# Kernel optimization log

Measured on AMD Instinct MI355X. Metric: run time of the kernel, lower is better.

The kernel has to match this reference:

```python
import jax, jax.numpy as jnp
import numpy as np

EMBED_DIM = 512
NUM_HEADS = 8
HEAD_DIM = EMBED_DIM // NUM_HEADS
B, S = 4, 2048


def setup_inputs() -> dict:
    key = jax.random.key(0)
    ks = jax.random.split(key, 9)
    scale = 1.0 / np.sqrt(EMBED_DIM)
    def lin(k):
        kw, kb = jax.random.split(k)
        W = jax.random.uniform(kw, (EMBED_DIM, EMBED_DIM), jnp.float32, -scale, scale)
        b = jax.random.uniform(kb, (EMBED_DIM,), jnp.float32, -scale, scale)
        return W, b
    Wq, bq = lin(ks[0])
    Wk, bk = lin(ks[1])
    Wv, bv = lin(ks[2])
    Wo, bo = lin(ks[3])
    x = jax.random.normal(ks[4], (B, S, EMBED_DIM), jnp.float32)
    return {"x": x, "Wq": Wq, "bq": bq, "Wk": Wk, "bk": bk,
            "Wv": Wv, "bv": bv, "Wo": Wo, "bo": bo}


def reference(x, Wq, bq, Wk, bk, Wv, bv, Wo, bo):
    # x: [B, S, E]. Linear uses y = x @ W^T + b (torch convention: W stored [out,in]).
    def split_heads(t):
        return t.reshape(B, S, NUM_HEADS, HEAD_DIM).transpose(0, 2, 1, 3)  # [B,H,S,D]
    q = split_heads(x @ Wq.T + bq)
    k = split_heads(x @ Wk.T + bk)
    v = split_heads(x @ Wv.T + bv)
    scores = jnp.einsum('bhsd,bhtd->bhst', q, k) / jnp.sqrt(jnp.float32(HEAD_DIM))
    attn_weights = jax.nn.softmax(scores, axis=-1)  # dropout is identity in eval mode
    attn_output = jnp.einsum('bhst,bhtd->bhsd', attn_weights, v)
    attn_output = attn_output.transpose(0, 2, 1, 3).reshape(B, S, EMBED_DIM)
    output = attn_output @ Wo.T + bo
    return output, attn_weights
```

## Files before the change

### kernel.cpp

```cpp
#include <hip/hip_runtime.h>
#include <stdint.h>

#define NB 4
#define NH 8
#define SS 2048
#define EE 512
#define DD 64
#define MM (NB*SS)
#define LDP 72
#define LDW 136

typedef __attribute__((ext_vector_type(8))) __bf16 bf16x8;
typedef __attribute__((ext_vector_type(8))) unsigned short ushort8;
typedef __attribute__((ext_vector_type(4))) unsigned short ushort4v;
typedef __attribute__((ext_vector_type(4))) float f32x4;

__device__ __forceinline__ uint16_t f2bf(float f) {
    union { float f; uint32_t u; } v; v.f = f;
    return (uint16_t)((v.u + 0x7fffu + ((v.u >> 16) & 1u)) >> 16);
}
__device__ __forceinline__ float bf2f(uint16_t h) {
    union { uint32_t u; float f; } v; v.u = ((uint32_t)h) << 16;
    return v.f;
}

__global__ __launch_bounds__(256) void split_all(
        const float* __restrict__ x,  const float* __restrict__ Wq,
        const float* __restrict__ Wk, const float* __restrict__ Wv,
        const float* __restrict__ Wo,
        uint16_t* __restrict__ xh, uint16_t* __restrict__ xl,
        uint16_t* __restrict__ wqkvh, uint16_t* __restrict__ wqkvl,
        uint16_t* __restrict__ woh, uint16_t* __restrict__ wol)
{
    const int tid = threadIdx.x;
    int b = blockIdx.x;
    const float* src; uint16_t* dh; uint16_t* dl; int i;
    if (b < 4096) { src = x; dh = xh; dl = xl; i = b*256 + tid; }
    else {
        b -= 4096;
        const int seg = b >> 8;
        i = (b & 255)*256 + tid;
        src = (seg == 0) ? Wq : (seg == 1) ? Wk : (seg == 2) ? Wv : Wo;
        if (seg < 3) { dh = wqkvh + (size_t)seg*262144; dl = wqkvl + (size_t)seg*262144; }
        else         { dh = woh; dl = wol; }
    }
    f32x4 v = reinterpret_cast<const f32x4*>(src)[i];
    ushort4v h, l;
#pragma unroll
    for (int j = 0; j < 4; j++) {
        uint16_t hh = f2bf(v[j]);
        h[j] = hh;
        l[j] = f2bf(v[j] - bf2f(hh));
    }
    reinterpret_cast<ushort4v*>(dh)[i] = h;
    reinterpret_cast<ushort4v*>(dl)[i] = l;
}

__global__ __launch_bounds__(256, 3)
void gemm_qkv(const uint16_t* __restrict__ Ah, const uint16_t* __restrict__ Al,
              const uint16_t* __restrict__ Bh, const uint16_t* __restrict__ Bl,
              const float* __restrict__ bq, const float* __restrict__ bk,
              const float* __restrict__ bv, float qscale,
              uint16_t* __restrict__ qh, uint16_t* __restrict__ ql,
              uint16_t* __restrict__ kh, uint16_t* __restrict__ kl,
              uint16_t* __restrict__ vh)
{
    __shared__ uint16_t sAh[64*64], sAl[64*64], sBh[128*64], sBl[128*64];
    const int t = threadIdx.x;
    const int lane = t & 63;
    const int wave = t >> 6;
    const int m0 = blockIdx.x * 64;
    const int n0 = blockIdx.y * 128;

    f32x4 zero = {0.f, 0.f, 0.f, 0.f};
    f32x4 acc[2][4];
#pragma unroll
    for (int i = 0; i < 2; i++)
#pragma unroll
        for (int j = 0; j < 4; j++) acc[i][j] = zero;

    const int sr = t >> 3;
    const int c8 = t & 7;
    const int sc = c8 * 8;
    const int dsw = ((c8 ^ (sr & 7)) << 3);
    const int l15 = lane & 15;
    const int l16 = lane >> 4;

    for (int k0 = 0; k0 < EE; k0 += 64) {
#pragma unroll
        for (int p = 0; p < 2; p++) {
            const int row = sr + 32 * p;
            const size_t ga = (size_t)(m0 + row) * EE + k0 + sc;
            const int o = row*64 + dsw;
            *reinterpret_cast<ushort8*>(&sAh[o]) = *reinterpret_cast<const ushort8*>(&Ah[ga]);
            *reinterpret_cast<ushort8*>(&sAl[o]) = *reinterpret_cast<const ushort8*>(&Al[ga]);
        }
#pragma unroll
        for (int p = 0; p < 4; p++) {
            const int row = sr + 32 * p;
            const size_t gb = (size_t)(n0 + row) * EE + k0 + sc;
            const int o = row*64 + dsw;
            *reinterpret_cast<ushort8*>(&sBh[o]) = *reinterpret_cast<const ushort8*>(&Bh[gb]);
            *reinterpret_cast<ushort8*>(&sBl[o]) = *reinterpret_cast<const ushort8*>(&Bl[gb]);
        }
        __syncthreads();
        const int mw = (wave >> 1) * 32;
        const int nw = (wave & 1) * 64;
#pragma unroll
        for (int ks = 0; ks < 2; ks++) {
            const int kc = ks*4 + l16;
            bf16x8 fah[2], fal[2], fbh[4], fbl[4];
#pragma unroll
            for (int i = 0; i < 2; i++) {
                const int ar = mw + 16*i + l15;
                const int ra = ar*64 + ((kc ^ (ar & 7)) << 3);
                fah[i] = *reinterpret_cast<const bf16x8*>(&sAh[ra]);
                fal[i] = *reinterpret_cast<const bf16x8*>(&sAl[ra]);
            }
#pragma unroll
            for (int j = 0; j < 4; j++) {
                const int br = nw + 16*j + l15;
                const int rb = br*64 + ((kc ^ (br & 7)) << 3);
                fbh[j] = *reinterpret_cast<const bf16x8*>(&sBh[rb]);
                fbl[j] = *reinterpret_cast<const bf16x8*>(&sBl[rb]);
            }
#pragma unroll
            for (int i = 0; i < 2; i++)
#pragma unroll
                for (int j = 0; j < 4; j++) {
                    acc[i][j] = __builtin_amdgcn_mfma_f32_16x16x32_bf16(fah[i], fbh[j], acc[i][j], 0, 0, 0);
                    acc[i][j] = __builtin_amdgcn_mfma_f32_16x16x32_bf16(fah[i], fbl[j], acc[i][j], 0, 0, 0);
                    acc[i][j] = __builtin_amdgcn_mfma_f32_16x16x32_bf16(fal[i], fbh[j], acc[i][j], 0, 0, 0);
                }
        }
        __syncthreads();
    }

    const int mw = (wave >> 1) * 32;
    const int nw = (wave & 1) * 64;
#pragma unroll
    for (int j = 0; j < 4; j++) {
        const int col = n0 + nw + 16*j + l15;
        const int seg = col >> 9;
        const int c   = col & 511;
        const float bias = (seg == 0 ? bq : (seg == 1 ? bk : bv))[c];
        const float scale = (seg == 0) ? qscale : 1.0f;
        const int h = c >> 6, d = c & 63;
#pragma unroll
        for (int i = 0; i < 2; i++) {
            const int rowb = m0 + mw + 16*i + (l16 << 2);
#pragma unroll
            for (int r4 = 0; r4 < 4; r4++) {
                const int m = rowb + r4;
                const float val = (acc[i][j][r4] + bias) * scale;
                const int bb = m >> 11, s = m & (SS-1);
                const size_t idx = (((size_t)(bb*NH + h)) * SS + s) * DD + d;
                const uint16_t hi = f2bf(val);
                if (seg == 0)      { qh[idx] = hi; ql[idx] = f2bf(val - bf2f(hi)); }
                else if (seg == 1) { kh[idx] = hi; kl[idx] = f2bf(val - bf2f(hi)); }
                else               { vh[idx] = hi; }
            }
        }
    }
}

__global__ __launch_bounds__(256, 3)
void gemm_out(const uint16_t* __restrict__ Ah, const uint16_t* __restrict__ Al,
              const uint16_t* __restrict__ Bh, const uint16_t* __restrict__ Bl,
              const float* __restrict__ bo, float* __restrict__ Of)
{
    __shared__ uint16_t sAh[64*64], sAl[64*64], sBh[128*64], sBl[128*64];
    const int t = threadIdx.x;
    const int lane = t & 63;
    const int wave = t >> 6;
    const int m0 = blockIdx.x * 64;
    const int n0 = blockIdx.y * 128;

    f32x4 zero = {0.f, 0.f, 0.f, 0.f};
    f32x4 acc[2][4];
#pragma unroll
    for (int i = 0; i < 2; i++)
#pragma unroll
        for (int j = 0; j < 4; j++) acc[i][j] = zero;

    const int sr = t >> 3;
    const int c8 = t & 7;
    const int sc = c8 * 8;
    const int dsw = ((c8 ^ (sr & 7)) << 3);
    const int l15 = lane & 15;
    const int l16 = lane >> 4;

    for (int k0 = 0; k0 < EE; k0 += 64) {
#pragma unroll
        for (int p = 0; p < 2; p++) {
            const int row = sr + 32 * p;
            const size_t ga = (size_t)(m0 + row) * EE + k0 + sc;
            const int o = row*64 + dsw;
            *reinterpret_cast<ushort8*>(&sAh[o]) = *reinterpret_cast<const ushort8*>(&Ah[ga]);
            *reinterpret_cast<ushort8*>(&sAl[o]) = *reinterpret_cast<const ushort8*>(&Al[ga]);
        }
#pragma unroll
        for (int p = 0; p < 4; p++) {
            const int row = sr + 32 * p;
            const size_t gb = (size_t)(n0 + row) * EE + k0 + sc;
            const int o = row*64 + dsw;
            *reinterpret_cast<ushort8*>(&sBh[o]) = *reinterpret_cast<const ushort8*>(&Bh[gb]);
            *reinterpret_cast<ushort8*>(&sBl[o]) = *reinterpret_cast<const ushort8*>(&Bl[gb]);
        }
        __syncthreads();
        const int mw = (wave >> 1) * 32;
        const int nw = (wave & 1) * 64;
#pragma unroll
        for (int ks = 0; ks < 2; ks++) {
            const int kc = ks*4 + l16;
            bf16x8 fah[2], fal[2], fbh[4], fbl[4];
#pragma unroll
            for (int i = 0; i < 2; i++) {
                const int ar = mw + 16*i + l15;
                const int ra = ar*64 + ((kc ^ (ar & 7)) << 3);
                fah[i] = *reinterpret_cast<const bf16x8*>(&sAh[ra]);
                fal[i] = *reinterpret_cast<const bf16x8*>(&sAl[ra]);
            }
#pragma unroll
            for (int j = 0; j < 4; j++) {
                const int br = nw + 16*j + l15;
                const int rb = br*64 + ((kc ^ (br & 7)) << 3);
                fbh[j] = *reinterpret_cast<const bf16x8*>(&sBh[rb]);
                fbl[j] = *reinterpret_cast<const bf16x8*>(&sBl[rb]);
            }
#pragma unroll
            for (int i = 0; i < 2; i++)
#pragma unroll
                for (int j = 0; j < 4; j++) {
                    acc[i][j] = __builtin_amdgcn_mfma_f32_16x16x32_bf16(fah[i], fbh[j], acc[i][j], 0, 0, 0);
                    acc[i][j] = __builtin_amdgcn_mfma_f32_16x16x32_bf16(fah[i], fbl[j], acc[i][j], 0, 0, 0);
                    acc[i][j] = __builtin_amdgcn_mfma_f32_16x16x32_bf16(fal[i], fbh[j], acc[i][j], 0, 0, 0);
                }
        }
        __syncthreads();
    }

    const int mw = (wave >> 1) * 32;
    const int nw = (wave & 1) * 64;
#pragma unroll
    for (int j = 0; j < 4; j++) {
        const int col = n0 + nw + 16*j + l15;
        const float bv = bo[col];
#pragma unroll
        for (int i = 0; i < 2; i++) {
            const int rowb = m0 + mw + 16*i + (l16 << 2);
#pragma unroll
            for (int r4 = 0; r4 < 4; r4++)
                Of[(size_t)(rowb + r4) * EE + col] = acc[i][j][r4] + bv;
        }
    }
}

__global__ __launch_bounds__(256, 2)
void attn_fused(const uint16_t* __restrict__ Qh, const uint16_t* __restrict__ Ql,
                const uint16_t* __restrict__ Kh, const uint16_t* __restrict__ Kl,
                const uint16_t* __restrict__ Vh,
                float* __restrict__ attn,
                uint16_t* __restrict__ Oh, uint16_t* __restrict__ Ol)
{
    __shared__ __align__(16) uint16_t smem[36864];
    uint16_t* bufA = smem;
    uint16_t* bufB = smem + 18432;

    const int t = threadIdx.x, lane = t & 63, wave = t >> 6;
    const int qt = blockIdx.x, bh = blockIdx.y;
    const size_t hb = (size_t)bh * SS * DD;
    const uint16_t* kbh = Kh + hb;
    const uint16_t* kbl = Kl + hb;
    const uint16_t* vbs = Vh + hb;

    const int l15 = lane & 15;
    const int l16 = lane >> 4;
    const int sr = t >> 3;
    const int sc = (t & 7) * 8;

    ushort8 krh[4], krl[4];
    auto kload_hi = [&](int kt) {
#pragma unroll
        for (int p = 0; p < 4; p++) {
            const size_t g = (size_t)(kt*128 + sr + 32*p) * DD + sc;
            krh[p] = *reinterpret_cast<const ushort8*>(&kbh[g]);
        }
    };
    auto kwrite_hi = [&](uint16_t* buf) {
#pragma unroll
        for (int p = 0; p < 4; p++) {
            const int o = (sr + 32*p)*LDP + sc;
            *reinterpret_cast<ushort8*>(&buf[o]) = krh[p];
        }
    };
    auto kload = [&](int kt) {
#pragma unroll
        for (int p = 0; p < 4; p++) {
            const size_t g = (size_t)(kt*128 + sr + 32*p) * DD + sc;
            krh[p] = *reinterpret_cast<const ushort8*>(&kbh[g]);
            krl[p] = *reinterpret_cast<const ushort8*>(&kbl[g]);
        }
    };
    auto kwrite = [&](uint16_t* buf) {
#pragma unroll
        for (int p = 0; p < 4; p++) {
            const int o = (sr + 32*p)*LDP + sc;
            *reinterpret_cast<ushort8*>(&buf[o]) = krh[p];
            *reinterpret_cast<ushort8*>(&buf[9216 + o]) = krl[p];
        }
    };

    bf16x8 qfh[2][2], qfl[2][2];
#pragma unroll
    for (int i = 0; i < 2; i++)
#pragma unroll
        for (int ks = 0; ks < 2; ks++) {
            const size_t qa = hb + (size_t)(qt*128 + wave*32 + 16*i + l15) * DD + ks*32 + l16*8;
            qfh[i][ks] = *reinterpret_cast<const bf16x8*>(&Qh[qa]);
            qfl[i][ks] = *reinterpret_cast<const bf16x8*>(&Ql[qa]);
        }

    f32x4 zero = {0.f, 0.f, 0.f, 0.f};
    f32x4 lsum[2] = {zero, zero};

    kload_hi(0);
#pragma unroll 1
    for (int kt = 0; kt < 16; kt++) {
        uint16_t* buf = (kt & 1) ? bufB : bufA;
        kwrite_hi(buf);
        if (kt < 15) kload_hi(kt + 1);
        __syncthreads();

        f32x4 accs[2][8];
#pragma unroll
        for (int i = 0; i < 2; i++)
#pragma unroll
            for (int j = 0; j < 8; j++) accs[i][j] = zero;

#pragma unroll
        for (int ks = 0; ks < 2; ks++) {
            const int kk = ks*32 + l16*8;
#pragma unroll
            for (int j = 0; j < 8; j++) {
                const int rb = (16*j + l15) * LDP + kk;
                bf16x8 fbh = *reinterpret_cast<const bf16x8*>(&buf[rb]);
#pragma unroll
                for (int i = 0; i < 2; i++)
                    accs[i][j] = __builtin_amdgcn_mfma_f32_16x16x32_bf16(qfh[i][ks], fbh, accs[i][j], 0, 0, 0);
            }
        }

#pragma unroll
        for (int i = 0; i < 2; i++)
#pragma unroll
            for (int j = 0; j < 8; j++)
#pragma unroll
                for (int r = 0; r < 4; r++)
                    lsum[i][r] += __builtin_amdgcn_exp2f(accs[i][j][r]);
    }

    f32x4 iv[2];
#pragma unroll
    for (int i = 0; i < 2; i++)
#pragma unroll
        for (int r = 0; r < 4; r++) {
            float s = lsum[i][r];
#pragma unroll
            for (int o = 1; o < 16; o <<= 1) s += __shfl_xor(s, o);
            iv[i][r] = 1.0f / s;
        }

    f32x4 acco[2][4];
#pragma unroll
    for (int i = 0; i < 2; i++)
#pragma unroll
        for (int j = 0; j < 4; j++) acco[i][j] = zero;

    float* wbase = attn + ((size_t)bh * SS + qt*128) * SS;

    const int pk = t & 63;
    const int dbase = (t >> 6) * 16;
    ushort8 vr[2][2];
    auto vload = [&](int kt) {
#pragma unroll
        for (int u = 0; u < 2; u++)
#pragma unroll
            for (int s = 0; s < 2; s++)
                vr[u][s] = *reinterpret_cast<const ushort8*>(
                    &vbs[(size_t)(kt*128 + 2*pk + s) * DD + dbase + u*8]);
    };
    auto vwrite = [&](uint16_t* vbufp) {
#pragma unroll
        for (int u = 0; u < 2; u++)
#pragma unroll
            for (int e = 0; e < 8; e++) {
                const int d = dbase + u*8 + e;
                const uint32_t pack = (uint32_t)(unsigned short)vr[u][0][e]
                                    | ((uint32_t)(unsigned short)vr[u][1][e] << 16);
                *reinterpret_cast<uint32_t*>(&vbufp[d*LDW + 2*pk]) = pack;
            }
    };

    __syncthreads();

    kload(0); vload(0);
#pragma unroll 1
    for (int kt = 0; kt < 16; kt++) {
        kwrite(bufA);
        vwrite(bufB);
        __syncthreads();

        f32x4 accs[2][8];
#pragma unroll
        for (int i = 0; i < 2; i++)
#pragma unroll
            for (int j = 0; j < 8; j++) accs[i][j] = zero;
#pragma unroll
        for (int ks = 0; ks < 2; ks++) {
            const int kk = ks*32 + l16*8;
#pragma unroll
            for (int j = 0; j < 8; j++) {
                const int rb = (16*j + l15) * LDP + kk;
                bf16x8 fbh = *reinterpret_cast<const bf16x8*>(&bufA[rb]);
                bf16x8 fbl = *reinterpret_cast<const bf16x8*>(&bufA[9216 + rb]);
#pragma unroll
                for (int i = 0; i < 2; i++) {
                    accs[i][j] = __builtin_amdgcn_mfma_f32_16x16x32_bf16(qfh[i][ks], fbh, accs[i][j], 0, 0, 0);
                    accs[i][j] = __builtin_amdgcn_mfma_f32_16x16x32_bf16(qfh[i][ks], fbl, accs[i][j], 0, 0, 0);
                    accs[i][j] = __builtin_amdgcn_mfma_f32_16x16x32_bf16(qfl[i][ks], fbh, accs[i][j], 0, 0, 0);
                }
            }
        }

        if (kt < 15) { kload(kt + 1); vload(kt + 1); }

#pragma unroll
        for (int i = 0; i < 2; i++)
#pragma unroll
            for (int j = 0; j < 8; j++)
#pragma unroll
                for (int r = 0; r < 4; r++)
                    accs[i][j][r] = __builtin_amdgcn_exp2f(accs[i][j][r]) * iv[i][r];

        __syncthreads();

#pragma unroll
        for (int i = 0; i < 2; i++)
#pragma unroll
            for (int r = 0; r < 4; r++) {
                const int row = wave*32 + 16*i + l16*4 + r;
#pragma unroll
                for (int j = 0; j < 8; j++)
                    bufA[row*LDW + l15 + 16*j] = f2bf(accs[i][j][r]);
            }
        __syncthreads();

#pragma unroll
        for (int i = 0; i < 2; i++)
#pragma unroll
            for (int r = 0; r < 4; r++) {
                const int row = wave*32 + 16*i + l16*4 + r;
                float* wout = wbase + (size_t)row * SS + kt*128 + l15;
#pragma unroll
                for (int j = 0; j < 8; j++)
                    __builtin_nontemporal_store(accs[i][j][r], &wout[16*j]);
            }

#pragma unroll
        for (int ks = 0; ks < 4; ks++) {
            const int kk = ks*32 + l16*8;
            bf16x8 wa[2], vbf[4];
#pragma unroll
            for (int i = 0; i < 2; i++)
                wa[i] = *reinterpret_cast<const bf16x8*>(&bufA[(wave*32 + 16*i + l15)*LDW + kk]);
#pragma unroll
            for (int j = 0; j < 4; j++)
                vbf[j] = *reinterpret_cast<const bf16x8*>(&bufB[(16*j + l15)*LDW + kk]);
#pragma unroll
            for (int i = 0; i < 2; i++)
#pragma unroll
                for (int j = 0; j < 4; j++)
                    acco[i][j] = __builtin_amdgcn_mfma_f32_16x16x32_bf16(wa[i], vbf[j], acco[i][j], 0, 0, 0);
        }
        __syncthreads();
    }

    const int b = bh >> 3, h = bh & 7;
#pragma unroll
    for (int i = 0; i < 2; i++)
#pragma unroll
        for (int j = 0; j < 4; j++)
#pragma unroll
            for (int r4 = 0; r4 < 4; r4++) {
                const int srow = qt*128 + wave*32 + 16*i + (l16 << 2) + r4;
                const int col = h*64 + 16*j + l15;
                const size_t idx = ((size_t)b * SS + srow) * (size_t)EE + col;
                const float val = acco[i][j][r4];
                const uint16_t hh = f2bf(val);
                Oh[idx] = hh;
                Ol[idx] = f2bf(val - bf2f(hh));
            }
}

extern "C" void kernel_launch(void* const* d_in, const int* in_sizes, int n_in,
                              void* d_out, int out_size, void* d_ws, size_t ws_size,
                              hipStream_t stream)
{
    const float* x  = (const float*)d_in[0];
    const float* Wq = (const float*)d_in[1];
    const float* bq = (const float*)d_in[2];
    const float* Wk = (const float*)d_in[3];
    const float* bk = (const float*)d_in[4];
    const float* Wv = (const float*)d_in[5];
    const float* bv = (const float*)d_in[6];
    const float* Wo = (const float*)d_in[7];
    const float* bo = (const float*)d_in[8];

    float* outF = (float*)d_out;
    float* attn = outF + (size_t)MM * EE;

    const size_t NXE = (size_t)MM * EE;
    const size_t NW  = (size_t)EE * EE;
    uint16_t* p = (uint16_t*)d_ws;
    uint16_t* xh    = p;          p += NXE;
    uint16_t* xl    = p;          p += NXE;
    uint16_t* wqkvh = p;          p += 3*NW;
    uint16_t* wqkvl = p;          p += 3*NW;
    uint16_t* woh   = p;          p += NW;
    uint16_t* wol   = p;          p += NW;
    uint16_t* qh    = p;          p += NXE;
    uint16_t* ql    = p;          p += NXE;
    uint16_t* kh    = p;          p += NXE;
    uint16_t* kl    = p;          p += NXE;
    uint16_t* vh    = p;          p += NXE;
    uint16_t* ah    = p;          p += NXE;
    uint16_t* al    = p;          p += NXE;

    split_all<<<4096 + 4*256, 256, 0, stream>>>(x, Wq, Wk, Wv, Wo,
                                                xh, xl, wqkvh, wqkvl, woh, wol);

    const float qscale = 0.125f * 1.44269504088896340736f;
    gemm_qkv<<<dim3(MM/64, (3*EE)/128), 256, 0, stream>>>(
        xh, xl, wqkvh, wqkvl, bq, bk, bv, qscale, qh, ql, kh, kl, vh);

    attn_fused<<<dim3(SS/128, NB*NH), 256, 0, stream>>>(qh, ql, kh, kl, vh, attn, ah, al);

    gemm_out<<<dim3(MM/64, EE/128), 256, 0, stream>>>(ah, al, woh, wol, bo, outF);
}
```

Measured before the change: 244.9 us.

## Double attention query tile to 256 rows with 512-thread blocks sharing K/V tiles

The attention kernel now processes 256 query rows per block with 8 waves instead of 128 rows with 4 waves. Each K and V tile loaded into LDS is reused by twice as many query rows, halving global K/V traffic per query. The LDS layout gets dedicated regions for K, the attention-weight tile and transposed V, which lets one barrier per iteration be removed, while an extra barrier is added to the first pass. Grid size halves to 256 blocks and occupancy drops to one block per CU, which risks poorer latency hiding and load balance.

Result: slower. 285.8 us (+16.7%).

```diff
diff --git a/kernel.cpp b/kernel.cpp
--- a/kernel.cpp
+++ b/kernel.cpp
@@ -256,16 +256,17 @@
     }
 }
 
-__global__ __launch_bounds__(256, 2)
+__global__ __launch_bounds__(512, 1)
 void attn_fused(const uint16_t* __restrict__ Qh, const uint16_t* __restrict__ Ql,
                 const uint16_t* __restrict__ Kh, const uint16_t* __restrict__ Kl,
                 const uint16_t* __restrict__ Vh,
                 float* __restrict__ attn,
                 uint16_t* __restrict__ Oh, uint16_t* __restrict__ Ol)
 {
-    __shared__ __align__(16) uint16_t smem[36864];
-    uint16_t* bufA = smem;
-    uint16_t* bufB = smem + 18432;
+    __shared__ __align__(16) uint16_t smem[61952];
+    uint16_t* kbuf = smem;
+    uint16_t* wlds = smem + 18432;
+    uint16_t* vlds = smem + 53248;
 
     const int t = threadIdx.x, lane = t & 63, wave = t >> 6;
     const int qt = blockIdx.x, bh = blockIdx.y;
@@ -279,35 +280,31 @@
     const int sr = t >> 3;
     const int sc = (t & 7) * 8;
 
-    ushort8 krh[4], krl[4];
+    ushort8 krh[2], krl[2];
     auto kload_hi = [&](int kt) {
 #pragma unroll
-        for (int p = 0; p < 4; p++) {
-            const size_t g = (size_t)(kt*128 + sr + 32*p) * DD + sc;
-            krh[p] = *reinterpret_cast<const ushort8*>(&kbh[g]);
-        }
+        for (int p = 0; p < 2; p++)
+            krh[p] = *reinterpret_cast<const ushort8*>(&kbh[(size_t)(kt*128 + sr + 64*p) * DD + sc]);
     };
     auto kwrite_hi = [&](uint16_t* buf) {
 #pragma unroll
-        for (int p = 0; p < 4; p++) {
-            const int o = (sr + 32*p)*LDP + sc;
-            *reinterpret_cast<ushort8*>(&buf[o]) = krh[p];
-        }
+        for (int p = 0; p < 2; p++)
+            *reinterpret_cast<ushort8*>(&buf[(sr + 64*p)*LDP + sc]) = krh[p];
     };
     auto kload = [&](int kt) {
 #pragma unroll
-        for (int p = 0; p < 4; p++) {
-            const size_t g = (size_t)(kt*128 + sr + 32*p) * DD + sc;
+        for (int p = 0; p < 2; p++) {
+            const size_t g = (size_t)(kt*128 + sr + 64*p) * DD + sc;
             krh[p] = *reinterpret_cast<const ushort8*>(&kbh[g]);
             krl[p] = *reinterpret_cast<const ushort8*>(&kbl[g]);
         }
     };
-    auto kwrite = [&](uint16_t* buf) {
-#pragma unroll
-        for (int p = 0; p < 4; p++) {
-            const int o = (sr + 32*p)*LDP + sc;
-            *reinterpret_cast<ushort8*>(&buf[o]) = krh[p];
-            *reinterpret_cast<ushort8*>(&buf[9216 + o]) = krl[p];
+    auto kwrite = [&]() {
+#pragma unroll
+        for (int p = 0; p < 2; p++) {
+            const int o = (sr + 64*p)*LDP + sc;
+            *reinterpret_cast<ushort8*>(&kbuf[o]) = krh[p];
+            *reinterpret_cast<ushort8*>(&kbuf[9216 + o]) = krl[p];
         }
     };
 
@@ -316,7 +313,7 @@
     for (int i = 0; i < 2; i++)
 #pragma unroll
         for (int ks = 0; ks < 2; ks++) {
-            const size_t qa = hb + (size_t)(qt*128 + wave*32 + 16*i + l15) * DD + ks*32 + l16*8;
+            const size_t qa = hb + (size_t)(qt*256 + wave*32 + 16*i + l15) * DD + ks*32 + l16*8;
             qfh[i][ks] = *reinterpret_cast<const bf16x8*>(&Qh[qa]);
             qfl[i][ks] = *reinterpret_cast<const bf16x8*>(&Ql[qa]);
         }
@@ -327,7 +324,7 @@
     kload_hi(0);
 #pragma unroll 1
     for (int kt = 0; kt < 16; kt++) {
-        uint16_t* buf = (kt & 1) ? bufB : bufA;
+        uint16_t* buf = (kt & 1) ? wlds : kbuf;
         kwrite_hi(buf);
         if (kt < 15) kload_hi(kt + 1);
         __syncthreads();
@@ -358,6 +355,7 @@
 #pragma unroll
                 for (int r = 0; r < 4; r++)
                     lsum[i][r] += __builtin_amdgcn_exp2f(accs[i][j][r]);
+        __syncthreads();
     }
 
     f32x4 iv[2];
@@ -377,29 +375,25 @@
 #pragma unroll
         for (int j = 0; j < 4; j++) acco[i][j] = zero;
 
-    float* wbase = attn + ((size_t)bh * SS + qt*128) * SS;
+    float* wbase = attn + ((size_t)bh * SS + qt*256) * SS;
 
     const int pk = t & 63;
-    const int dbase = (t >> 6) * 16;
-    ushort8 vr[2][2];
+    const int dg = t >> 6;
+    ushort8 vr[2];
     auto vload = [&](int kt) {
 #pragma unroll
-        for (int u = 0; u < 2; u++)
-#pragma unroll
-            for (int s = 0; s < 2; s++)
-                vr[u][s] = *reinterpret_cast<const ushort8*>(
-                    &vbs[(size_t)(kt*128 + 2*pk + s) * DD + dbase + u*8]);
+        for (int s = 0; s < 2; s++)
+            vr[s] = *reinterpret_cast<const ushort8*>(
+                &vbs[(size_t)(kt*128 + 2*pk + s) * DD + dg*8]);
     };
-    auto vwrite = [&](uint16_t* vbufp) {
-#pragma unroll
-        for (int u = 0; u < 2; u++)
-#pragma unroll
-            for (int e = 0; e < 8; e++) {
-                const int d = dbase + u*8 + e;
-                const uint32_t pack = (uint32_t)(unsigned short)vr[u][0][e]
-                                    | ((uint32_t)(unsigned short)vr[u][1][e] << 16);
-                *reinterpret_cast<uint32_t*>(&vbufp[d*LDW + 2*pk]) = pack;
-            }
+    auto vwrite = [&]() {
+#pragma unroll
+        for (int e = 0; e < 8; e++) {
+            const int d = dg*8 + e;
+            const uint32_t pack = (uint32_t)(unsigned short)vr[0][e]
+                                | ((uint32_t)(unsigned short)vr[1][e] << 16);
+            *reinterpret_cast<uint32_t*>(&vlds[d*LDW + 2*pk]) = pack;
+        }
     };
 
     __syncthreads();
@@ -407,8 +401,8 @@
     kload(0); vload(0);
 #pragma unroll 1
     for (int kt = 0; kt < 16; kt++) {
-        kwrite(bufA);
-        vwrite(bufB);
+        kwrite();
+        vwrite();
         __syncthreads();
 
         f32x4 accs[2][8];
@@ -422,8 +416,8 @@
 #pragma unroll
             for (int j = 0; j < 8; j++) {
                 const int rb = (16*j + l15) * LDP + kk;
-                bf16x8 fbh = *reinterpret_cast<const bf16x8*>(&bufA[rb]);
-                bf16x8 fbl = *reinterpret_cast<const bf16x8*>(&bufA[9216 + rb]);
+                bf16x8 fbh = *reinterpret_cast<const bf16x8*>(&kbuf[rb]);
+                bf16x8 fbl = *reinterpret_cast<const bf16x8*>(&kbuf[9216 + rb]);
 #pragma unroll
                 for (int i = 0; i < 2; i++) {
                     accs[i][j] = __builtin_amdgcn_mfma_f32_16x16x32_bf16(qfh[i][ks], fbh, accs[i][j], 0, 0, 0);
@@ -443,8 +437,6 @@
                 for (int r = 0; r < 4; r++)
                     accs[i][j][r] = __builtin_amdgcn_exp2f(accs[i][j][r]) * iv[i][r];
 
-        __syncthreads();
-
 #pragma unroll
         for (int i = 0; i < 2; i++)
 #pragma unroll
@@ -452,7 +444,7 @@
                 const int row = wave*32 + 16*i + l16*4 + r;
 #pragma unroll
                 for (int j = 0; j < 8; j++)
-                    bufA[row*LDW + l15 + 16*j] = f2bf(accs[i][j][r]);
+                    wlds[row*LDW + l15 + 16*j] = f2bf(accs[i][j][r]);
             }
         __syncthreads();
 
@@ -473,10 +465,10 @@
             bf16x8 wa[2], vbf[4];
 #pragma unroll
             for (int i = 0; i < 2; i++)
-                wa[i] = *reinterpret_cast<const bf16x8*>(&bufA[(wave*32 + 16*i + l15)*LDW + kk]);
+                wa[i] = *reinterpret_cast<const bf16x8*>(&wlds[(wave*32 + 16*i + l15)*LDW + kk]);
 #pragma unroll
             for (int j = 0; j < 4; j++)
-                vbf[j] = *reinterpret_cast<const bf16x8*>(&bufB[(16*j + l15)*LDW + kk]);
+                vbf[j] = *reinterpret_cast<const bf16x8*>(&vlds[(16*j + l15)*LDW + kk]);
 #pragma unroll
             for (int i = 0; i < 2; i++)
 #pragma unroll
@@ -493,7 +485,7 @@
         for (int j = 0; j < 4; j++)
 #pragma unroll
             for (int r4 = 0; r4 < 4; r4++) {
-                const int srow = qt*128 + wave*32 + 16*i + (l16 << 2) + r4;
+                const int srow = qt*256 + wave*32 + 16*i + (l16 << 2) + r4;
                 const int col = h*64 + 16*j + l15;
                 const size_t idx = ((size_t)b * SS + srow) * (size_t)EE + col;
                 const float val = acco[i][j][r4];
@@ -544,7 +536,7 @@
     gemm_qkv<<<dim3(MM/64, (3*EE)/128), 256, 0, stream>>>(
         xh, xl, wqkvh, wqkvl, bq, bk, bv, qscale, qh, ql, kh, kl, vh);
 
-    attn_fused<<<dim3(SS/128, NB*NH), 256, 0, stream>>>(qh, ql, kh, kl, vh, attn, ah, al);
+    attn_fused<<<dim3(SS/256, NB*NH), 512, 0, stream>>>(qh, ql, kh, kl, vh, attn, ah, al);
 
     gemm_out<<<dim3(MM/64, EE/128), 256, 0, stream>>>(ah, al, woh, wol, bo, outF);
 }
```
